# Kernel tuning notes

Hardware: AMD Instinct MI355X
Metric: run time of the kernel (lower is better)

Reference implementation:

```python
import jax, jax.numpy as jnp
import numpy as np

VOCAB = 50000
CELL = 512          # cell_size
EMB = CELL - 1      # embedding dim per docstring
LAYERS = 4
NUM_LABELS = 64
B, T = 64, 256


def setup_inputs() -> dict:
    key = jax.random.key(0)
    ks = jax.random.split(key, 10)
    word_ids = jax.random.randint(ks[0], (B, T), 0, VOCAB, dtype=jnp.int32)
    predicate_ids = jax.random.randint(ks[1], (B, T), 0, 2, dtype=jnp.int32)
    mask = jax.random.randint(ks[2], (B, T), 0, 2, dtype=jnp.int32)
    embeddings = jax.random.normal(ks[3], (VOCAB, EMB), dtype=jnp.float32) * 0.1
    # all layers have input dim == CELL (emb + predicate channel == CELL)
    Ws = jax.random.normal(ks[4], (LAYERS, CELL, 4 * CELL), dtype=jnp.float32) * 0.05
    Us = jax.random.normal(ks[5], (LAYERS, CELL, 4 * CELL), dtype=jnp.float32) * 0.05
    bs = jnp.zeros((LAYERS, 4 * CELL), dtype=jnp.float32)
    Wout = jax.random.normal(ks[6], (CELL, NUM_LABELS), dtype=jnp.float32) * 0.05
    bout = jnp.zeros((NUM_LABELS,), dtype=jnp.float32)
    return {"word_ids": word_ids, "predicate_ids": predicate_ids, "mask": mask,
            "embeddings": embeddings, "Ws": Ws, "Us": Us, "bs": bs,
            "Wout": Wout, "bout": bout}


def _lstm_layer(x, m, W, U, b):
    """x: [B,T,D], m: [B,T] bool. Keras semantics: masked steps carry h,c
    (output at masked step repeats previous output, which equals h)."""
    Bq, Tq, _ = x.shape
    H = U.shape[0]
    pre = jnp.einsum('btd,dk->btk', x, W) + b          # [B,T,4H] input GEMM hoisted
    pre_t = jnp.transpose(pre, (1, 0, 2))              # [T,B,4H] time-major
    m_t = jnp.transpose(m, (1, 0))                     # [T,B]

    def step(carry, inp):
        h, c = carry
        p, mt = inp
        z = p + h @ U                                  # [B,4H]
        i, f, g, o = jnp.split(z, 4, axis=-1)          # keras gate order i,f,c,o
        i = jax.nn.sigmoid(i); f = jax.nn.sigmoid(f)
        g = jnp.tanh(g); o = jax.nn.sigmoid(o)
        c_new = f * c + i * g
        h_new = o * jnp.tanh(c_new)
        keep = mt[:, None]
        h = jnp.where(keep, h_new, h)
        c = jnp.where(keep, c_new, c)
        return (h, c), h

    h0 = jnp.zeros((Bq, H), dtype=x.dtype)
    c0 = jnp.zeros((Bq, H), dtype=x.dtype)
    _, hs = jax.lax.scan(step, (h0, c0), (pre_t, m_t))
    return jnp.transpose(hs, (1, 0, 2))                # [B,T,H]


def reference(word_ids, predicate_ids, mask, embeddings, Ws, Us, bs, Wout, bout):
    # embed + concat predicate indicator channel -> [B,T,CELL]
    x = embeddings[word_ids]
    x = jnp.concatenate([x, predicate_ids[..., None].astype(x.dtype)], axis=-1)
    m = mask.astype(bool)
    for layer in range(Ws.shape[0]):
        go_back = (layer % 2 == 1)
        xi = jnp.flip(x, axis=1) if go_back else x
        mi = jnp.flip(m, axis=1) if go_back else m
        # keras go_backwards does NOT re-reverse outputs when return_sequences=True
        x = _lstm_layer(xi, mi, Ws[layer], Us[layer], bs[layer])
    H = Wout.shape[0]
    encoded_2d = x.reshape(-1, H)                      # [B*T, H]
    logits = encoded_2d @ Wout + bout                  # [B*T, num_labels]
    return logits
```

## Files before the change

kernel.cpp:

```cpp
#include <hip/hip_runtime.h>
#include <math.h>

#define TQ 256
#define DQ 512
#define GQ 2048

typedef __attribute__((ext_vector_type(8))) short bf16x8;
typedef __attribute__((ext_vector_type(4))) float f32x4;
typedef __attribute__((ext_vector_type(4))) unsigned u32x4;

__device__ __forceinline__ unsigned f2bf(float x) {
    unsigned u = __builtin_bit_cast(unsigned, x);
    return (u + 0x7fffu + ((u >> 16) & 1u)) >> 16;
}
__device__ __forceinline__ float bf2f(unsigned s) {
    return __builtin_bit_cast(float, s << 16);
}
__device__ __forceinline__ float sigf(float x) { return 1.f / (1.f + __expf(-x)); }
__device__ __forceinline__ float tanhfast(float x) { return 1.f - 2.f / (__expf(2.f * x) + 1.f); }

__device__ __forceinline__ bf16x8 frag_load16(const unsigned short* p) {
    bf16x8 r;
    asm volatile("global_load_dwordx4 %0, %1, off sc0" : "=v"(r) : "v"(p));
    return r;
}

__global__ __launch_bounds__(256) void k_embed(const int* __restrict__ wid,
                                               const int* __restrict__ pid,
                                               const float* __restrict__ emb,
                                               float* __restrict__ xT) {
    __shared__ float Ls[64][65];
    int t = blockIdx.x;
    int d0 = blockIdx.y * 64;
    int tid = threadIdx.x;
    int l = tid & 63;
    int grp = tid >> 6;
#pragma unroll 4
    for (int bb = 0; bb < 16; ++bb) {
        int b = grp * 16 + bb;
        int d = d0 + l;
        float v;
        if (d < 511) v = emb[(size_t)wid[b * TQ + t] * 511 + d];
        else         v = (float)pid[b * TQ + t];
        Ls[l][b] = v;
    }
    __syncthreads();
#pragma unroll 4
    for (int dd = 0; dd < 16; ++dd) {
        int dl = grp * 16 + dd;
        xT[((size_t)t * DQ + d0 + dl) * 64 + l] = Ls[dl][l];
    }
}

__global__ __launch_bounds__(256) void k_convX(const float* __restrict__ xT,
                                               unsigned short* __restrict__ Xh,
                                               unsigned short* __restrict__ Xl) {
    int idx = blockIdx.x * 256 + threadIdx.x;
    int b = idx & 63;
    int d = (idx >> 6) & 511;
    int t = idx >> 15;
    float v = xT[idx];
    unsigned hi = f2bf(v);
    unsigned lo = f2bf(v - bf2f(hi));
    size_t wi = (((size_t)(1 + t) * 4 + (b >> 4)) * 16 + (d >> 5)) * 512 +
                (((d >> 3) & 3) * 16 + (b & 15)) * 8 + (d & 7);
    Xh[wi] = (unsigned short)hi;
    Xl[wi] = (unsigned short)lo;
}

__global__ __launch_bounds__(256) void k_convW(const float* __restrict__ Ws,
                                               unsigned short* __restrict__ Wh,
                                               unsigned short* __restrict__ Wl) {
    int idx = blockIdx.x * 256 + threadIdx.x;
    int c = idx & 2047;
    int d = (idx >> 11) & 511;
    int lay = idx >> 20;
    float v = Ws[idx];
    unsigned hi = f2bf(v);
    unsigned lo = f2bf(v - bf2f(hi));
    size_t wi = (((size_t)lay * 128 + (c >> 4)) * 16 + (d >> 5)) * 512 +
                (((d >> 3) & 3) * 16 + (c & 15)) * 8 + (d & 7);
    Wh[wi] = (unsigned short)hi;
    Wl[wi] = (unsigned short)lo;
}

__global__ __launch_bounds__(256) void k_convU(const float* __restrict__ Us,
                                               unsigned short* __restrict__ Uh,
                                               unsigned short* __restrict__ Ul) {
    int idx = blockIdx.x * 256 + threadIdx.x;
    int c = idx & 2047;
    int k = (idx >> 11) & 511;
    int lay = idx >> 20;
    float v = Us[idx];
    unsigned hi = f2bf(v);
    unsigned lo = f2bf(v - bf2f(hi));
    int g = c >> 9;
    int o = (c >> 3) & 63;
    int jl = c & 7;
    int nt = g >> 1;
    int n = (g & 1) * 8 + jl;
    size_t wi = ((((size_t)lay * 64 + o) * 16 + (k >> 5)) * 2 + nt) * 512 +
                (((k >> 3) & 3) * 16 + n) * 8 + (k & 7);
    Uh[wi] = (unsigned short)hi;
    Ul[wi] = (unsigned short)lo;
}

__global__ __launch_bounds__(512, 1) void k_fused(
    const unsigned short* __restrict__ Uh, const unsigned short* __restrict__ Ul,
    const unsigned short* __restrict__ Wh, const unsigned short* __restrict__ Wl,
    const unsigned short* __restrict__ Xih, const unsigned short* __restrict__ Xil,
    unsigned short* __restrict__ Xoh, unsigned short* __restrict__ Xol,
    float* __restrict__ preF, const int* __restrict__ mask,
    const float* __restrict__ bias, float* __restrict__ xT32,
    unsigned* __restrict__ bar, int flip, int writeX)
{
    __shared__ char ldsraw[81920];
    int wg = blockIdx.x;
    int tid = threadIdx.x;
    int w = tid >> 6, l = tid & 63;
    unsigned* pre_cnt = bar + 1024;

    if (wg >= 128) {
        float* stage = (float*)ldsraw + w * (16 * 68);
        int q = wg - 128;
        for (int T = q; T < 4096; T += 128) {
            int sl = T >> 4, cg = T & 15;
            int t_in = flip ? (255 - sl) : sl;
            int ct = cg * 8 + w;
            size_t xb = (size_t)(1 + t_in) * 32768 + (size_t)l * 8;
            f32x4 acc[4];
            f32x4 zv = {0.f, 0.f, 0.f, 0.f};
#pragma unroll
            for (int bt = 0; bt < 4; ++bt) acc[bt] = zv;

#pragma unroll 2
            for (int kt = 0; kt < 16; ++kt) {
                size_t wa = ((size_t)ct * 16 + kt) * 512 + l * 8;
                bf16x8 ah = *(const bf16x8*)(Wh + wa);
                bf16x8 al = *(const bf16x8*)(Wl + wa);
                bf16x8 bh[4], bo[4];
#pragma unroll
                for (int bt = 0; bt < 4; ++bt) {
                    size_t a = xb + (size_t)(bt * 16 + kt) * 512;
                    bh[bt] = *(const bf16x8*)(Xih + a);
                    bo[bt] = *(const bf16x8*)(Xil + a);
                }
#pragma unroll
                for (int bt = 0; bt < 4; ++bt) {
                    acc[bt] = __builtin_amdgcn_mfma_f32_16x16x32_bf16(ah, bh[bt], acc[bt], 0, 0, 0);
                    acc[bt] = __builtin_amdgcn_mfma_f32_16x16x32_bf16(al, bh[bt], acc[bt], 0, 0, 0);
                    acc[bt] = __builtin_amdgcn_mfma_f32_16x16x32_bf16(ah, bo[bt], acc[bt], 0, 0, 0);
                }
            }
#pragma unroll
            for (int bt = 0; bt < 4; ++bt)
#pragma unroll
                for (int r = 0; r < 4; ++r)
                    stage[((l >> 4) * 4 + r) * 68 + bt * 16 + (l & 15)] = acc[bt][r];
#pragma unroll
            for (int p = 0; p < 4; ++p) {
                int cr = p * 4 + (l >> 4);
                float bv = bias[ct * 16 + cr];
                f32x4 v = *(f32x4*)&stage[cr * 68 + (l & 15) * 4];
                v[0] += bv; v[1] += bv; v[2] += bv; v[3] += bv;
                float* dst = &preF[((size_t)sl * GQ + ct * 16 + cr) * 64 + (l & 15) * 4];
                asm volatile("global_store_dwordx4 %0, %1, off sc0 sc1" :: "v"(dst), "v"(v));
            }
            __syncthreads();
            if (tid == 0)
                __hip_atomic_fetch_add(&pre_cnt[sl], 1u, __ATOMIC_RELAXED,
                                       __HIP_MEMORY_SCOPE_AGENT);
        }
        return;
    }

    int o = wg >> 1, half = wg & 1;
    int kh = w >> 1, mq = w & 1;
    int mt = half * 2 + mq;
    float* part = (float*)ldsraw;
    unsigned* hlds = (unsigned*)(ldsraw + 16896);

    bf16x8 BH[4][2], BL[4][2];
#pragma unroll
    for (int kt2 = 0; kt2 < 4; ++kt2)
#pragma unroll
        for (int nt = 0; nt < 2; ++nt) {
            size_t a = (((size_t)o * 16 + kh * 4 + kt2) * 2 + nt) * 512 + l * 8;
            BH[kt2][nt] = *(const bf16x8*)(Uh + a);
            BL[kt2][nt] = *(const bf16x8*)(Ul + a);
        }

    int u8 = (tid >> 5) & 7;
    int bl = tid & 31;
    int jglob = o * 8 + u8;
    int bglob = half * 32 + bl;
    bool fin = tid < 256;

    float creg = 0.f, hpre = 0.f;
    float pzv[4];
    int maskv = 0;

    if (tid == 0) {
        while (__hip_atomic_load(&pre_cnt[0], __ATOMIC_RELAXED,
                                 __HIP_MEMORY_SCOPE_AGENT) < 16u)
            __builtin_amdgcn_s_sleep(1);
    }
    __syncthreads();
    if (fin) {
        int t0 = flip ? 255 : 0;
        maskv = mask[bglob * TQ + t0];
#pragma unroll
        for (int g = 0; g < 4; ++g)
            pzv[g] = preF[(size_t)(g * 512 + jglob) * 64 + bglob];
    }

    for (int sl = 0; sl < 256; ++sl) {
        if (l < 16) {
            const unsigned* fp = bar + ((((kh * 16 + l) << 1) | half) << 3);
            while (__hip_atomic_load(fp, __ATOMIC_RELAXED,
                                     __HIP_MEMORY_SCOPE_AGENT) < (unsigned)sl)
                __builtin_amdgcn_s_sleep(1);
        }
        if (tid == 256 && sl < 255) {
            while (__hip_atomic_load(&pre_cnt[sl + 1], __ATOMIC_RELAXED,
                                     __HIP_MEMORY_SCOPE_AGENT) < 16u)
                __builtin_amdgcn_s_sleep(1);
        }

        bf16x8 AH[4], AL[4];
        size_t fb = (size_t)sl * 32768 + (size_t)(mt * 16 + kh * 4) * 512 + (size_t)l * 8;
#pragma unroll
        for (int kt2 = 0; kt2 < 4; ++kt2) {
            AH[kt2] = frag_load16(Xoh + fb + kt2 * 512);
            AL[kt2] = frag_load16(Xol + fb + kt2 * 512);
        }
        asm volatile("s_waitcnt vmcnt(0)" ::: "memory");
        __builtin_amdgcn_sched_barrier(0);

        f32x4 acc0 = {0.f, 0.f, 0.f, 0.f};
        f32x4 acc1 = {0.f, 0.f, 0.f, 0.f};
#pragma unroll
        for (int kt2 = 0; kt2 < 4; ++kt2) {
            acc0 = __builtin_amdgcn_mfma_f32_16x16x32_bf16(AH[kt2], BH[kt2][0], acc0, 0, 0, 0);
            acc1 = __builtin_amdgcn_mfma_f32_16x16x32_bf16(AH[kt2], BH[kt2][1], acc1, 0, 0, 0);
            acc0 = __builtin_amdgcn_mfma_f32_16x16x32_bf16(AL[kt2], BH[kt2][0], acc0, 0, 0, 0);
            acc1 = __builtin_amdgcn_mfma_f32_16x16x32_bf16(AL[kt2], BH[kt2][1], acc1, 0, 0, 0);
            acc0 = __builtin_amdgcn_mfma_f32_16x16x32_bf16(AH[kt2], BL[kt2][0], acc0, 0, 0, 0);
            acc1 = __builtin_amdgcn_mfma_f32_16x16x32_bf16(AH[kt2], BL[kt2][1], acc1, 0, 0, 0);
        }

#pragma unroll
        for (int r = 0; r < 4; ++r) {
            int col = mq * 16 + (l >> 4) * 4 + r;
            part[((kh * 2 + 0) * 16 + (l & 15)) * 33 + col] = acc0[r];
            part[((kh * 2 + 1) * 16 + (l & 15)) * 33 + col] = acc1[r];
        }
        __syncthreads();

        if (fin) {
            float z[4];
#pragma unroll
            for (int g = 0; g < 4; ++g) {
                float zz = pzv[g];
#pragma unroll
                for (int k2 = 0; k2 < 4; ++k2)
                    zz += part[((k2 * 2 + (g >> 1)) * 16 + (g & 1) * 8 + u8) * 33 + bl];
                z[g] = zz;
            }
            float ig = sigf(z[0]);
            float fg = sigf(z[1]);
            float gg = tanhfast(z[2]);
            float og = sigf(z[3]);
            float cn = fg * creg + ig * gg;
            float hn = og * tanhfast(cn);
            bool mk = maskv != 0;
            float ho = mk ? hn : hpre;
            creg = mk ? cn : creg;
            hpre = ho;
            if (writeX)
                xT32[((size_t)sl * DQ + jglob) * 64 + bglob] = ho;
            unsigned hi = f2bf(ho);
            unsigned lo = f2bf(ho - bf2f(hi));
            hlds[u8 * 32 + bl] = hi | (lo << 16);
        }
        __syncthreads();

        if (w == 7) {
            int plane = l >> 5, b2 = l & 31;
            int bg = half * 32 + b2;
            unsigned v[8];
#pragma unroll
            for (int u = 0; u < 8; ++u) v[u] = hlds[u * 32 + b2];
            u32x4 d;
            if (plane == 0) {
#pragma unroll
                for (int i = 0; i < 4; ++i)
                    d[i] = (v[2 * i] & 0xffffu) | (v[2 * i + 1] << 16);
            } else {
#pragma unroll
                for (int i = 0; i < 4; ++i)
                    d[i] = (v[2 * i] >> 16) | (v[2 * i + 1] & 0xffff0000u);
            }
            size_t wi = (((size_t)(sl + 1) * 4 + (bg >> 4)) * 16 + (o >> 2)) * 512 +
                        ((o & 3) * 16 + (bg & 15)) * 8;
            unsigned short* dst = (plane ? Xol : Xoh) + wi;
            asm volatile("global_store_dwordx4 %0, %1, off sc0 sc1" :: "v"(dst), "v"(d));
            asm volatile("s_waitcnt vmcnt(0)" ::: "memory");
            if (l == 0)
                __hip_atomic_store(&bar[wg * 8], (unsigned)(sl + 1),
                                   __ATOMIC_RELAXED, __HIP_MEMORY_SCOPE_AGENT);
        }

        if (fin && sl < 255) {
            int t1 = flip ? (254 - sl) : (sl + 1);
            maskv = mask[bglob * TQ + t1];
#pragma unroll
            for (int g = 0; g < 4; ++g)
                pzv[g] = preF[((size_t)(sl + 1) * GQ + g * 512 + jglob) * 64 + bglob];
        }
    }
}

__global__ __launch_bounds__(256) void k_out(const float* __restrict__ xT,
                                             const float* __restrict__ Wo,
                                             const float* __restrict__ bo,
                                             float* __restrict__ out) {
    __shared__ float WoL[64 * 64];
    int t = blockIdx.x;
    int tid = threadIdx.x;
    int b = tid & 63;
    int q = tid >> 6;
    float acc[16];
#pragma unroll
    for (int i = 0; i < 16; ++i) acc[i] = 0.f;

    for (int kc = 0; kc < 8; ++kc) {
        __syncthreads();
#pragma unroll
        for (int uu = 0; uu < 4; ++uu)
            *(float4*)&WoL[tid * 16 + uu * 4] =
                *(const float4*)&Wo[kc * 4096 + tid * 16 + uu * 4];
        __syncthreads();
        for (int kk = 0; kk < 64; ++kk) {
            float xv = xT[((size_t)t * DQ + kc * 64 + kk) * 64 + b];
#pragma unroll
            for (int uu = 0; uu < 4; ++uu) {
                float4 wv = *(const float4*)&WoL[kk * 64 + q * 16 + uu * 4];
                acc[uu * 4 + 0] += xv * wv.x;
                acc[uu * 4 + 1] += xv * wv.y;
                acc[uu * 4 + 2] += xv * wv.z;
                acc[uu * 4 + 3] += xv * wv.w;
            }
        }
    }
#pragma unroll
    for (int uu = 0; uu < 4; ++uu) {
        int n = q * 16 + uu * 4;
        float4 v = {acc[uu * 4 + 0] + bo[n + 0], acc[uu * 4 + 1] + bo[n + 1],
                    acc[uu * 4 + 2] + bo[n + 2], acc[uu * 4 + 3] + bo[n + 3]};
        *(float4*)&out[((size_t)(b * TQ + t)) * 64 + n] = v;
    }
}

extern "C" void kernel_launch(void* const* d_in, const int* in_sizes, int n_in,
                              void* d_out, int out_size, void* d_ws, size_t ws_size,
                              hipStream_t stream) {
    const int*   wid  = (const int*)d_in[0];
    const int*   pid  = (const int*)d_in[1];
    const int*   mask = (const int*)d_in[2];
    const float* emb  = (const float*)d_in[3];
    const float* Ws   = (const float*)d_in[4];
    const float* Us   = (const float*)d_in[5];
    const float* bs   = (const float*)d_in[6];
    const float* Wo   = (const float*)d_in[7];
    const float* bo   = (const float*)d_in[8];
    float* out = (float*)d_out;

    const size_t XFPLANE = (size_t)257 * 32768;
    char* p = (char*)d_ws;
    float* xRaw = (float*)p;                  p += 33554432;
    unsigned short* XFA = (unsigned short*)p; p += 2 * XFPLANE * 2;
    unsigned short* XFB = (unsigned short*)p; p += 2 * XFPLANE * 2;
    unsigned short* UFh = (unsigned short*)p; p += 8388608;
    unsigned short* UFl = (unsigned short*)p; p += 8388608;
    unsigned short* WFh = (unsigned short*)p; p += 8388608;
    unsigned short* WFl = (unsigned short*)p; p += 8388608;
    unsigned* bar = (unsigned*)p;             p += 8192;
    float* preF = (float*)p;

    k_convU<<<16384, 256, 0, stream>>>(Us, UFh, UFl);
    k_convW<<<16384, 256, 0, stream>>>(Ws, WFh, WFl);
    k_embed<<<dim3(TQ, 8), 256, 0, stream>>>(wid, pid, emb, xRaw);
    k_convX<<<32768, 256, 0, stream>>>(xRaw, XFA, XFA + XFPLANE);

    for (int layer = 0; layer < 4; ++layer) {
        int flip = layer & 1;
        int writeX = (layer == 3) ? 1 : 0;
        const float* bias = bs + (size_t)layer * GQ;
        const unsigned short* UFh_l = UFh + (size_t)layer * 1048576;
        const unsigned short* UFl_l = UFl + (size_t)layer * 1048576;
        const unsigned short* WFh_l = WFh + (size_t)layer * 1048576;
        const unsigned short* WFl_l = WFl + (size_t)layer * 1048576;
        unsigned short* Xi = (layer & 1) ? XFB : XFA;
        unsigned short* Xo = (layer & 1) ? XFA : XFB;

        hipMemsetAsync(Xo, 0, 65536, stream);
        hipMemsetAsync(Xo + XFPLANE, 0, 65536, stream);
        hipMemsetAsync(bar, 0, 8192, stream);

        k_fused<<<256, 512, 0, stream>>>(UFh_l, UFl_l, WFh_l, WFl_l,
                                         Xi, Xi + XFPLANE, Xo, Xo + XFPLANE,
                                         preF, mask, bias, xRaw, bar,
                                         flip, writeX);
    }

    k_out<<<TQ, 256, 0, stream>>>(xRaw, Wo, bo, out);
}
```

Baseline: 3.265 ms.

## Replace per-step global flag polling with dedicated waiter waves and LDS ready flags

Restructures the per-timestep synchronization of the persistent LSTM recurrence. Dedicated waves now poll the global barrier flags and the precompute counters and publish readiness through LDS volatile flags. Finisher waves exchange h across lanes with ds_bpermute instead of an LDS staging buffer plus a second __syncthreads. Completion is counted with an LDS atomic so only the last wave writes the global flag. It also splits the A-fragment waits so the hi-part MFMAs start before the lo loads land. The aim is to cut barrier latency on the serial critical path, at the risk of spin-wait hazards on volatile LDS and a changed flag layout (bar indexed half*64+o).

```diff
diff --git a/kernel.cpp b/kernel.cpp
--- a/kernel.cpp
+++ b/kernel.cpp
@@ -178,7 +178,9 @@
     int kh = w >> 1, mq = w & 1;
     int mt = half * 2 + mq;
     float* part = (float*)ldsraw;
-    unsigned* hlds = (unsigned*)(ldsraw + 16896);
+    volatile int* vReady    = (volatile int*)(ldsraw + 16896);
+    volatile int* vPreReady = (volatile int*)(ldsraw + 16900);
+    unsigned* dCnt = (unsigned*)(ldsraw + 16904);
 
     bf16x8 BH[4][2], BL[4][2];
 #pragma unroll
@@ -190,23 +192,28 @@
             BL[kt2][nt] = *(const bf16x8*)(Ul + a);
         }
 
-    int u8 = (tid >> 5) & 7;
-    int bl = tid & 31;
+    int u8 = l >> 3;
+    int bq = l & 7;
+    int bl = w * 8 + bq;
     int jglob = o * 8 + u8;
     int bglob = half * 32 + bl;
-    bool fin = tid < 256;
+    bool isFin = (w < 4);
 
     float creg = 0.f, hpre = 0.f;
     float pzv[4];
     int maskv = 0;
 
-    if (tid == 0) {
+    if (tid == 0) { *vReady = 0; *vPreReady = -1; *dCnt = 0u; }
+    __syncthreads();
+
+    if (w == 5 && l == 0) {
         while (__hip_atomic_load(&pre_cnt[0], __ATOMIC_RELAXED,
                                  __HIP_MEMORY_SCOPE_AGENT) < 16u)
             __builtin_amdgcn_s_sleep(1);
-    }
-    __syncthreads();
-    if (fin) {
+        *vPreReady = 0;
+    }
+    if (isFin) {
+        while (*vPreReady < 0) {}
         int t0 = flip ? 255 : 0;
         maskv = mask[bglob * TQ + t0];
 #pragma unroll
@@ -215,34 +222,31 @@
     }
 
     for (int sl = 0; sl < 256; ++sl) {
-        if (l < 16) {
-            const unsigned* fp = bar + ((((kh * 16 + l) << 1) | half) << 3);
-            while (__hip_atomic_load(fp, __ATOMIC_RELAXED,
-                                     __HIP_MEMORY_SCOPE_AGENT) < (unsigned)sl)
-                __builtin_amdgcn_s_sleep(1);
-        }
-        if (tid == 256 && sl < 255) {
-            while (__hip_atomic_load(&pre_cnt[sl + 1], __ATOMIC_RELAXED,
-                                     __HIP_MEMORY_SCOPE_AGENT) < 16u)
-                __builtin_amdgcn_s_sleep(1);
-        }
+        while (*vReady < sl) {}
 
         bf16x8 AH[4], AL[4];
         size_t fb = (size_t)sl * 32768 + (size_t)(mt * 16 + kh * 4) * 512 + (size_t)l * 8;
 #pragma unroll
-        for (int kt2 = 0; kt2 < 4; ++kt2) {
+        for (int kt2 = 0; kt2 < 4; ++kt2)
             AH[kt2] = frag_load16(Xoh + fb + kt2 * 512);
+#pragma unroll
+        for (int kt2 = 0; kt2 < 4; ++kt2)
             AL[kt2] = frag_load16(Xol + fb + kt2 * 512);
-        }
-        asm volatile("s_waitcnt vmcnt(0)" ::: "memory");
-        __builtin_amdgcn_sched_barrier(0);
 
         f32x4 acc0 = {0.f, 0.f, 0.f, 0.f};
         f32x4 acc1 = {0.f, 0.f, 0.f, 0.f};
+
+        asm volatile("s_waitcnt vmcnt(4)" ::: "memory");
+        __builtin_amdgcn_sched_barrier(0);
 #pragma unroll
         for (int kt2 = 0; kt2 < 4; ++kt2) {
             acc0 = __builtin_amdgcn_mfma_f32_16x16x32_bf16(AH[kt2], BH[kt2][0], acc0, 0, 0, 0);
             acc1 = __builtin_amdgcn_mfma_f32_16x16x32_bf16(AH[kt2], BH[kt2][1], acc1, 0, 0, 0);
+        }
+        asm volatile("s_waitcnt vmcnt(0)" ::: "memory");
+        __builtin_amdgcn_sched_barrier(0);
+#pragma unroll
+        for (int kt2 = 0; kt2 < 4; ++kt2) {
             acc0 = __builtin_amdgcn_mfma_f32_16x16x32_bf16(AL[kt2], BH[kt2][0], acc0, 0, 0, 0);
             acc1 = __builtin_amdgcn_mfma_f32_16x16x32_bf16(AL[kt2], BH[kt2][1], acc1, 0, 0, 0);
             acc0 = __builtin_amdgcn_mfma_f32_16x16x32_bf16(AH[kt2], BL[kt2][0], acc0, 0, 0, 0);
@@ -257,7 +261,7 @@
         }
         __syncthreads();
 
-        if (fin) {
+        if (isFin) {
             float z[4];
 #pragma unroll
             for (int g = 0; g < 4; ++g) {
@@ -279,44 +283,71 @@
             hpre = ho;
             if (writeX)
                 xT32[((size_t)sl * DQ + jglob) * 64 + bglob] = ho;
+
             unsigned hi = f2bf(ho);
             unsigned lo = f2bf(ho - bf2f(hi));
-            hlds[u8 * 32 + bl] = hi | (lo << 16);
-        }
-        __syncthreads();
-
-        if (w == 7) {
-            int plane = l >> 5, b2 = l & 31;
-            int bg = half * 32 + b2;
+            unsigned packed = hi | (lo << 16);
+
             unsigned v[8];
 #pragma unroll
-            for (int u = 0; u < 8; ++u) v[u] = hlds[u * 32 + b2];
-            u32x4 d;
-            if (plane == 0) {
-#pragma unroll
-                for (int i = 0; i < 4; ++i)
-                    d[i] = (v[2 * i] & 0xffffu) | (v[2 * i + 1] << 16);
-            } else {
-#pragma unroll
-                for (int i = 0; i < 4; ++i)
-                    d[i] = (v[2 * i] >> 16) | (v[2 * i + 1] & 0xffff0000u);
-            }
-            size_t wi = (((size_t)(sl + 1) * 4 + (bg >> 4)) * 16 + (o >> 2)) * 512 +
-                        ((o & 3) * 16 + (bg & 15)) * 8;
-            unsigned short* dst = (plane ? Xol : Xoh) + wi;
-            asm volatile("global_store_dwordx4 %0, %1, off sc0 sc1" :: "v"(dst), "v"(d));
+            for (int u = 0; u < 8; ++u)
+                v[u] = (unsigned)__builtin_amdgcn_ds_bpermute((u * 8 + bq) * 4, (int)packed);
+
+            if (l < 16) {
+                int p = l >> 3;
+                int b = w * 8 + (l & 7);
+                int bg = half * 32 + b;
+                u32x4 d;
+                if (p == 0) {
+#pragma unroll
+                    for (int i = 0; i < 4; ++i)
+                        d[i] = (v[2 * i] & 0xffffu) | (v[2 * i + 1] << 16);
+                } else {
+#pragma unroll
+                    for (int i = 0; i < 4; ++i)
+                        d[i] = (v[2 * i] >> 16) | (v[2 * i + 1] & 0xffff0000u);
+                }
+                size_t wi = (((size_t)(sl + 1) * 4 + (bg >> 4)) * 16 + (o >> 2)) * 512 +
+                            ((o & 3) * 16 + (bg & 15)) * 8;
+                unsigned short* dst = (p ? Xol : Xoh) + wi;
+                asm volatile("global_store_dwordx4 %0, %1, off sc0 sc1" :: "v"(dst), "v"(d));
+            }
             asm volatile("s_waitcnt vmcnt(0)" ::: "memory");
-            if (l == 0)
-                __hip_atomic_store(&bar[wg * 8], (unsigned)(sl + 1),
-                                   __ATOMIC_RELAXED, __HIP_MEMORY_SCOPE_AGENT);
-        }
-
-        if (fin && sl < 255) {
-            int t1 = flip ? (254 - sl) : (sl + 1);
-            maskv = mask[bglob * TQ + t1];
-#pragma unroll
-            for (int g = 0; g < 4; ++g)
-                pzv[g] = preF[((size_t)(sl + 1) * GQ + g * 512 + jglob) * 64 + bglob];
+            if (l == 0) {
+                unsigned old = atomicAdd(dCnt, 1u);
+                if (old == (unsigned)(sl * 4 + 3)) {
+                    unsigned* fdst = bar + half * 64 + o;
+                    unsigned fval = (unsigned)(sl + 1);
+                    asm volatile("global_store_dword %0, %1, off sc0 sc1" :: "v"(fdst), "v"(fval));
+                }
+            }
+            if (sl < 255) {
+                while (*vPreReady < sl + 1) {}
+                int t1 = flip ? (254 - sl) : (sl + 1);
+                maskv = mask[bglob * TQ + t1];
+#pragma unroll
+                for (int g = 0; g < 4; ++g)
+                    pzv[g] = preF[((size_t)(sl + 1) * GQ + g * 512 + jglob) * 64 + bglob];
+            }
+        } else if (w == 4) {
+            if (sl < 255) {
+                int tgt = sl + 1;
+                const unsigned* fp = bar + half * 64 + l;
+                int okv;
+                do {
+                    unsigned vv = __hip_atomic_load(fp, __ATOMIC_RELAXED,
+                                                    __HIP_MEMORY_SCOPE_AGENT);
+                    okv = (vv >= (unsigned)tgt);
+                } while (!__all(okv));
+                if (l == 0) *vReady = tgt;
+            }
+        } else if (w == 5) {
+            if (sl < 255 && l == 0) {
+                while (__hip_atomic_load(&pre_cnt[sl + 1], __ATOMIC_RELAXED,
+                                         __HIP_MEMORY_SCOPE_AGENT) < 16u)
+                    __builtin_amdgcn_s_sleep(1);
+                *vPreReady = sl + 1;
+            }
         }
     }
 }
```

Measured after the change: 5.378 ms. +64.7%, slower.
